# Kernel tuning notes

Hardware: AMD Instinct MI355X
Metric: run time of the kernel (lower is better)

The kernel has to match this reference:

```python
import jax, jax.numpy as jnp
import numpy as np

N_QUBITS = 12
FAST_DEPTH = 4
FAST_DECAY = 0.9
LATENT = 512
BATCH = 2048


def _apply_ry(state, theta, wire):
    # state: (B, 2**n) real; RY is a real rotation. PennyLane default.qubit:
    # wire 0 is the most-significant bit of the state index.
    B = state.shape[0]
    s = state.reshape(B, 1 << wire, 2, -1)
    h = theta * 0.5
    c = jnp.cos(h)[:, None, None]
    sn = jnp.sin(h)[:, None, None]
    s0, s1 = s[:, :, 0], s[:, :, 1]
    out = jnp.stack([c * s0 - sn * s1, sn * s0 + c * s1], axis=2)
    return out.reshape(state.shape)


def _apply_cnot_adjacent(state, wire):
    # CNOT with control=wire, target=wire+1 (nearest-neighbor chain)
    B = state.shape[0]
    s = state.reshape(B, 1 << wire, 2, 2, -1)
    out = jnp.stack([s[:, :, 0], s[:, :, 1, ::-1]], axis=2)
    return out.reshape(state.shape)


def _fwp_circuit(x, fast, n_qubits, n_outputs):
    # x: (B, n_qubits) RY encoding angles; fast: (B, depth, n_qubits)
    B = x.shape[0]
    dim = 1 << n_qubits
    # Hadamard layer on |0...0> -> uniform positive real amplitudes.
    state = jnp.full((B, dim), 2.0 ** (-n_qubits / 2), dtype=x.dtype)
    for w in range(n_qubits):
        state = _apply_ry(state, x[:, w], w)
    for layer in range(fast.shape[1]):
        for w in range(n_qubits - 1):
            state = _apply_cnot_adjacent(state, w)
        for w in range(n_qubits):
            state = _apply_ry(state, fast[:, layer, w], w)
    probs = state * state  # real state -> |amp|^2
    outs = []
    for w in range(n_outputs):
        p = probs.reshape(B, 1 << w, 2, -1)
        outs.append(p[:, :, 0].sum(axis=(1, 2)) - p[:, :, 1].sum(axis=(1, 2)))
    return jnp.stack(outs, axis=1)  # (B, n_outputs) PauliZ expvals


def setup_inputs() -> dict:
    key = jax.random.key(0)
    ks = jax.random.split(key, 6)
    n, depth, latent = N_QUBITS, FAST_DEPTH, LATENT
    return {
        "x_t": jax.random.normal(ks[0], (BATCH, n), jnp.float32),
        "fast_prev": jax.random.normal(ks[1], (BATCH, depth, n), jnp.float32) * 0.1,
        "W_enc": jax.random.normal(ks[2], (latent, n), jnp.float32) / np.sqrt(n).astype(np.float32),
        "b_enc": jnp.zeros((latent,), jnp.float32),
        "W_upd": jax.random.normal(ks[3], (depth * n, latent), jnp.float32) / np.sqrt(latent).astype(np.float32),
        "b_upd": jnp.zeros((depth * n,), jnp.float32),
        "W_ro": jax.random.normal(ks[4], (1, n), jnp.float32) / np.sqrt(n).astype(np.float32),
        "b_ro": jnp.zeros((1,), jnp.float32),
    }


def reference(x_t, fast_prev, W_enc, b_enc, W_upd, b_upd, W_ro, b_ro):
    latent = jnp.tanh(x_t @ W_enc.T + b_enc)
    delta = (latent @ W_upd.T + b_upd).reshape(x_t.shape[0], FAST_DEPTH, N_QUBITS)
    fast_next = FAST_DECAY * fast_prev + delta
    q_out = _fwp_circuit(x_t, fast_next, N_QUBITS, N_QUBITS)  # n_outputs = n_qubits
    y_t = q_out @ W_ro.T + b_ro
    return (y_t, fast_next)
```

## Files before the change

kernel.cpp:

```cpp
#include <hip/hip_runtime.h>

static constexpr int NQ    = 12;
static constexpr int DEPTH = 4;
static constexpr int LAT   = 512;
static constexpr int FAST  = DEPTH * NQ;
static constexpr float DECAY = 0.9f;


__device__ __forceinline__ float i2f(int x) { return __int_as_float(x); }

template<int M>
__device__ __forceinline__ float xpartner(float x, int lane) {
    int xi = __float_as_int(x);
    if constexpr (M == 1) {
        return i2f(__builtin_amdgcn_update_dpp(xi, xi, 0xB1, 0xF, 0xF, true));
    } else if constexpr (M == 2) {
        return i2f(__builtin_amdgcn_update_dpp(xi, xi, 0x4E, 0xF, 0xF, true));
    } else if constexpr (M == 4) {
        int t = __builtin_amdgcn_update_dpp(xi, xi, 0x141, 0xF, 0xF, true);
        return i2f(__builtin_amdgcn_update_dpp(t, t, 0x1B, 0xF, 0xF, true));
    } else if constexpr (M == 8) {
        return i2f(__builtin_amdgcn_update_dpp(xi, xi, 0x128, 0xF, 0xF, true));
    } else if constexpr (M == 16) {
#if __has_builtin(__builtin_amdgcn_permlane16_swap)
        auto r = __builtin_amdgcn_permlane16_swap((unsigned)xi, (unsigned)xi, false, false);
        return i2f((int)(r[0] ^ r[1]) ^ xi);
#else
        return __shfl_xor(x, 16, 64);
#endif
    } else {
#if __has_builtin(__builtin_amdgcn_permlane32_swap)
        auto r = __builtin_amdgcn_permlane32_swap((unsigned)xi, (unsigned)xi, false, false);
        return i2f((int)(r[0] ^ r[1]) ^ xi);
#else
        return __shfl_xor(x, 32, 64);
#endif
    }
}

template<int W>
__device__ __forceinline__ void ry_lane(float (&v)[64], int lane, float c, float s) {
    constexpr int M = 1 << (5 - W);
    float t = (lane & M) ? s : -s;
    #pragma unroll
    for (int r = 0; r < 64; r++) {
        float p = xpartner<M>(v[r], lane);
        v[r] = c * v[r] + t * p;
    }
}

template<int W>
__device__ __forceinline__ void ry_reg(float (&v)[64], float c, float s) {
    constexpr int S = 1 << (11 - W);
    #pragma unroll
    for (int r0 = 0; r0 < 64; r0++) {
        if ((r0 & S) == 0) {
            float a = v[r0];
            float b = v[r0 + S];
            v[r0]     = c * a - s * b;
            v[r0 + S] = s * a + c * b;
        }
    }
}

template<int W>
__device__ __forceinline__ void apply_cnot_reg(float (&v)[64]) {
    constexpr int CBS = 1 << (11 - W);
    constexpr int TBS = 1 << (10 - W);
    #pragma unroll
    for (int r = 0; r < 64; r++) {
        if ((r & CBS) != 0 && (r & TBS) == 0) {
            float tmp = v[r];
            v[r]       = v[r | TBS];
            v[r | TBS] = tmp;
        }
    }
}

template<int W>
__device__ __forceinline__ void cnot_reg_chain(float (&v)[64]) {
    if constexpr (W < 11) {
        apply_cnot_reg<W>(v);
        cnot_reg_chain<W + 1>(v);
    }
}

template<int W>
__device__ __forceinline__ void layer_rys(float (&v)[64], int lane, const float* ang) {
    if constexpr (W < 12) {
        float h = 0.5f * ang[W];
        float c = __cosf(h), s = __sinf(h);
        if constexpr (W < 6) ry_lane<W>(v, lane, c, s);
        else                 ry_reg<W>(v, c, s);
        layer_rys<W + 1>(v, lane, ang);
    }
}

__global__ __launch_bounds__(256, 2)
void fwp_kernel(const float* __restrict__ x_t,
                const float* __restrict__ fast_prev,
                const float* __restrict__ W_enc,
                const float* __restrict__ b_enc,
                const float* __restrict__ W_upd,
                const float* __restrict__ b_upd,
                const float* __restrict__ W_ro,
                const float* __restrict__ b_ro,
                float* __restrict__ out_y,
                float* __restrict__ out_fast) {
    const int lane = threadIdx.x & 63;
    const int wv   = threadIdx.x >> 6;
    const int b    = blockIdx.x * 4 + wv;

    __shared__ float s_lat[4][LAT];
    __shared__ float s_ang[4][FAST];

    float xr = (lane < NQ) ? x_t[b * NQ + lane] : 0.0f;
    float xa[NQ];
    #pragma unroll
    for (int k = 0; k < NQ; k++) xa[k] = __shfl(xr, k, 64);

    #pragma unroll
    for (int t = 0; t < LAT / 64; t++) {
        int j = lane + 64 * t;
        const float4* wr = (const float4*)(W_enc + j * NQ);
        float4 a0 = wr[0], a1 = wr[1], a2 = wr[2];
        float sum = b_enc[j]
            + a0.x * xa[0] + a0.y * xa[1] + a0.z * xa[2]  + a0.w * xa[3]
            + a1.x * xa[4] + a1.y * xa[5] + a1.z * xa[6]  + a1.w * xa[7]
            + a2.x * xa[8] + a2.y * xa[9] + a2.z * xa[10] + a2.w * xa[11];
        s_lat[wv][j] = tanhf(sum);
    }
    __syncthreads();

    if (lane < FAST) {
        const float4* wr = (const float4*)(W_upd + lane * LAT);
        const float4* lr = (const float4*)(s_lat[wv]);
        float sum = b_upd[lane];
        #pragma unroll 16
        for (int j = 0; j < LAT / 4; j++) {
            float4 w4 = wr[j];
            float4 l4 = lr[j];
            sum += w4.x * l4.x + w4.y * l4.y + w4.z * l4.z + w4.w * l4.w;
        }
        float ang = DECAY * fast_prev[b * FAST + lane] + sum;
        s_ang[wv][lane] = ang;
        out_fast[b * FAST + lane] = ang;
    }
    __syncthreads();

    float g0[NQ], g1[NQ];
    #pragma unroll
    for (int w = 0; w < NQ; w++) {
        float h = 0.5f * xa[w];
        float c = __cosf(h), s = __sinf(h);
        g0[w] = (c - s) * 0.70710678118654752f;
        g1[w] = (c + s) * 0.70710678118654752f;
    }
    float L = 1.0f;
    #pragma unroll
    for (int w = 0; w < 6; w++)
        L *= ((lane >> (5 - w)) & 1) ? g1[w] : g0[w];

    float v[64];
    v[0] = L;
    #pragma unroll
    for (int w = 6; w < NQ; w++) {
        const int S = 1 << (11 - w);
        #pragma unroll
        for (int r = 0; r < 64; r += 2 * S) {
            v[r + S] = v[r] * g1[w];
            v[r]     = v[r] * g0[w];
        }
    }

    int csrc = lane;
    #pragma unroll
    for (int w = 4; w >= 0; w--)
        csrc ^= ((csrc >> (5 - w)) & 1) << (4 - w);
    const int csrc4 = csrc << 2;

    #pragma unroll 1
    for (int layer = 0; layer < DEPTH; layer++) {
        #pragma unroll
        for (int r = 0; r < 64; r++)
            v[r] = i2f(__builtin_amdgcn_ds_bpermute(csrc4, __float_as_int(v[r])));
        bool c5 = (lane & 1) != 0;
        #pragma unroll
        for (int r0 = 0; r0 < 32; r0++) {
            float a = v[r0], bb = v[r0 + 32];
            v[r0]      = c5 ? bb : a;
            v[r0 + 32] = c5 ? a : bb;
        }
        cnot_reg_chain<6>(v);
        layer_rys<0>(v, lane, &s_ang[wv][layer * NQ]);
    }

    float tot = 0.0f, pw[6] = {0, 0, 0, 0, 0, 0};
    #pragma unroll
    for (int r = 0; r < 64; r++) {
        float p = v[r] * v[r];
        tot += p;
        pw[0] += (r & 32) ? -p : p;
        pw[1] += (r & 16) ? -p : p;
        pw[2] += (r & 8)  ? -p : p;
        pw[3] += (r & 4)  ? -p : p;
        pw[4] += (r & 2)  ? -p : p;
        pw[5] += (r & 1)  ? -p : p;
    }
    float sl = 0.0f;
    #pragma unroll
    for (int w = 0; w < 6; w++) {
        float c = W_ro[w];
        sl += ((lane >> (5 - w)) & 1) ? -c : c;
    }
    float y = sl * tot;
    #pragma unroll
    for (int k = 0; k < 6; k++) y += W_ro[6 + k] * pw[k];
    #pragma unroll
    for (int m = 32; m >= 1; m >>= 1) y += __shfl_xor(y, m, 64);
    if (lane == 0) out_y[b] = y + b_ro[0];
}

extern "C" void kernel_launch(void* const* d_in, const int* in_sizes, int n_in,
                              void* d_out, int out_size, void* d_ws, size_t ws_size,
                              hipStream_t stream) {
    const float* x_t       = (const float*)d_in[0];
    const float* fast_prev = (const float*)d_in[1];
    const float* W_enc     = (const float*)d_in[2];
    const float* b_enc     = (const float*)d_in[3];
    const float* W_upd     = (const float*)d_in[4];
    const float* b_upd     = (const float*)d_in[5];
    const float* W_ro      = (const float*)d_in[6];
    const float* b_ro      = (const float*)d_in[7];
    float* out = (float*)d_out;

    fwp_kernel<<<2048 / 4, 256, 0, stream>>>(x_t, fast_prev, W_enc, b_enc,
                                             W_upd, b_upd, W_ro, b_ro,
                                             out , out + 2048 );
}
```

Baseline: 126.3 us.

## Use packed v2f math for RY gates, one wave per block, precomputed trig

Rewrites the RY rotation loops to use two-wide float vectors so the compiler can emit packed FMA instructions (v_pk_fma_f32) on CDNA. Switches from four waves per 256-thread block to one 64-thread block per batch element, shrinking shared memory and making __syncthreads cheaper. Moves the cos/sin of the fast-weight angles into the update stage, stored in shared memory and loaded per layer. Packed math may add register pressure or extra moves, and smaller blocks raise the block count and per-block launch overhead.

```diff
diff --git a/kernel.cpp b/kernel.cpp
--- a/kernel.cpp
+++ b/kernel.cpp
@@ -5,6 +5,8 @@
 static constexpr int LAT   = 512;
 static constexpr int FAST  = DEPTH * NQ;
 static constexpr float DECAY = 0.9f;
+
+using v2f = __attribute__((ext_vector_type(2))) float;
 
 
 __device__ __forceinline__ float i2f(int x) { return __int_as_float(x); }
@@ -42,23 +44,44 @@
 __device__ __forceinline__ void ry_lane(float (&v)[64], int lane, float c, float s) {
     constexpr int M = 1 << (5 - W);
     float t = (lane & M) ? s : -s;
-    #pragma unroll
-    for (int r = 0; r < 64; r++) {
-        float p = xpartner<M>(v[r], lane);
-        v[r] = c * v[r] + t * p;
+    v2f cc = {c, c}, tt = {t, t};
+    #pragma unroll
+    for (int k = 0; k < 32; k++) {
+        float p0 = xpartner<M>(v[2 * k],     lane);
+        float p1 = xpartner<M>(v[2 * k + 1], lane);
+        v2f vv = {v[2 * k], v[2 * k + 1]};
+        v2f pp = {p0, p1};
+        vv = cc * vv + tt * pp;
+        v[2 * k]     = vv.x;
+        v[2 * k + 1] = vv.y;
     }
 }
 
 template<int W>
 __device__ __forceinline__ void ry_reg(float (&v)[64], float c, float s) {
     constexpr int S = 1 << (11 - W);
-    #pragma unroll
-    for (int r0 = 0; r0 < 64; r0++) {
-        if ((r0 & S) == 0) {
-            float a = v[r0];
-            float b = v[r0 + S];
-            v[r0]     = c * a - s * b;
-            v[r0 + S] = s * a + c * b;
+    if constexpr (S >= 2) {
+        v2f cc = {c, c}, ss = {s, s};
+        #pragma unroll
+        for (int r0 = 0; r0 < 64; r0 += 2) {
+            if ((r0 & S) == 0) {
+                v2f a = {v[r0],     v[r0 + 1]};
+                v2f b = {v[r0 + S], v[r0 + S + 1]};
+                v2f na = cc * a - ss * b;
+                v2f nb = ss * a + cc * b;
+                v[r0]         = na.x;  v[r0 + 1]     = na.y;
+                v[r0 + S]     = nb.x;  v[r0 + S + 1] = nb.y;
+            }
+        }
+    } else {
+        v2f cs = {c, s}, nsc = {-s, c};
+        #pragma unroll
+        for (int r0 = 0; r0 < 64; r0 += 2) {
+            float a = v[r0], b = v[r0 + 1];
+            v2f aa = {a, a}, bb = {b, b};
+            v2f res = cs * aa + nsc * bb;
+            v[r0]     = res.x;
+            v[r0 + 1] = res.y;
         }
     }
 }
@@ -86,17 +109,16 @@
 }
 
 template<int W>
-__device__ __forceinline__ void layer_rys(float (&v)[64], int lane, const float* ang) {
+__device__ __forceinline__ void layer_rys(float (&v)[64], int lane,
+                                          const float* lc, const float* ls) {
     if constexpr (W < 12) {
-        float h = 0.5f * ang[W];
-        float c = __cosf(h), s = __sinf(h);
-        if constexpr (W < 6) ry_lane<W>(v, lane, c, s);
-        else                 ry_reg<W>(v, c, s);
-        layer_rys<W + 1>(v, lane, ang);
-    }
-}
-
-__global__ __launch_bounds__(256, 2)
+        if constexpr (W < 6) ry_lane<W>(v, lane, lc[W], ls[W]);
+        else                 ry_reg<W>(v, lc[W], ls[W]);
+        layer_rys<W + 1>(v, lane, lc, ls);
+    }
+}
+
+__global__ __launch_bounds__(64, 2)
 void fwp_kernel(const float* __restrict__ x_t,
                 const float* __restrict__ fast_prev,
                 const float* __restrict__ W_enc,
@@ -107,12 +129,11 @@
                 const float* __restrict__ b_ro,
                 float* __restrict__ out_y,
                 float* __restrict__ out_fast) {
-    const int lane = threadIdx.x & 63;
-    const int wv   = threadIdx.x >> 6;
-    const int b    = blockIdx.x * 4 + wv;
-
-    __shared__ float s_lat[4][LAT];
-    __shared__ float s_ang[4][FAST];
+    const int lane = threadIdx.x;
+    const int b    = blockIdx.x;
+
+    __shared__ __align__(16) float s_lat[LAT];
+    __shared__ float s_c[FAST], s_s[FAST];
 
     float xr = (lane < NQ) ? x_t[b * NQ + lane] : 0.0f;
     float xa[NQ];
@@ -128,13 +149,13 @@
             + a0.x * xa[0] + a0.y * xa[1] + a0.z * xa[2]  + a0.w * xa[3]
             + a1.x * xa[4] + a1.y * xa[5] + a1.z * xa[6]  + a1.w * xa[7]
             + a2.x * xa[8] + a2.y * xa[9] + a2.z * xa[10] + a2.w * xa[11];
-        s_lat[wv][j] = tanhf(sum);
+        s_lat[j] = tanhf(sum);
     }
     __syncthreads();
 
     if (lane < FAST) {
         const float4* wr = (const float4*)(W_upd + lane * LAT);
-        const float4* lr = (const float4*)(s_lat[wv]);
+        const float4* lr = (const float4*)(s_lat);
         float sum = b_upd[lane];
         #pragma unroll 16
         for (int j = 0; j < LAT / 4; j++) {
@@ -143,16 +164,18 @@
             sum += w4.x * l4.x + w4.y * l4.y + w4.z * l4.z + w4.w * l4.w;
         }
         float ang = DECAY * fast_prev[b * FAST + lane] + sum;
-        s_ang[wv][lane] = ang;
         out_fast[b * FAST + lane] = ang;
+        float hh = 0.5f * ang;
+        s_c[lane] = __cosf(hh);
+        s_s[lane] = __sinf(hh);
     }
     __syncthreads();
 
     float g0[NQ], g1[NQ];
     #pragma unroll
     for (int w = 0; w < NQ; w++) {
-        float h = 0.5f * xa[w];
-        float c = __cosf(h), s = __sinf(h);
+        float hh = 0.5f * xa[w];
+        float c = __cosf(hh), s = __sinf(hh);
         g0[w] = (c - s) * 0.70710678118654752f;
         g1[w] = (c + s) * 0.70710678118654752f;
     }
@@ -181,6 +204,12 @@
 
     #pragma unroll 1
     for (int layer = 0; layer < DEPTH; layer++) {
+        float lc[NQ], ls[NQ];
+        #pragma unroll
+        for (int w = 0; w < NQ; w++) {
+            lc[w] = s_c[layer * NQ + w];
+            ls[w] = s_s[layer * NQ + w];
+        }
         #pragma unroll
         for (int r = 0; r < 64; r++)
             v[r] = i2f(__builtin_amdgcn_ds_bpermute(csrc4, __float_as_int(v[r])));
@@ -192,7 +221,7 @@
             v[r0 + 32] = c5 ? a : bb;
         }
         cnot_reg_chain<6>(v);
-        layer_rys<0>(v, lane, &s_ang[wv][layer * NQ]);
+        layer_rys<0>(v, lane, lc, ls);
     }
 
     float tot = 0.0f, pw[6] = {0, 0, 0, 0, 0, 0};
@@ -234,7 +263,7 @@
     const float* b_ro      = (const float*)d_in[7];
     float* out = (float*)d_out;
 
-    fwp_kernel<<<2048 / 4, 256, 0, stream>>>(x_t, fast_prev, W_enc, b_enc,
-                                             W_upd, b_upd, W_ro, b_ro,
-                                             out , out + 2048 );
-}
+    fwp_kernel<<<2048, 64, 0, stream>>>(x_t, fast_prev, W_enc, b_enc,
+                                        W_upd, b_upd, W_ro, b_ro,
+                                        out , out + 2048 );
+}
```

Result: no change. 125.0 us (-1.1%).
